# Kernel tuning notes

Measured on AMD Instinct MI355X. Metric: run time of the kernel, lower is better.

The kernel has to match this reference:

```python
import jax, jax.numpy as jnp
import numpy as np

N_NODES = 100000
N_EDGES = 2000000
EPS = 1e-8


def setup_inputs() -> dict:
    key = jax.random.key(0)
    k1, k2 = jax.random.split(key)
    node_positions = jax.random.normal(k1, (1, N_NODES, 2), dtype=jnp.float32) * 10.0
    adjacency = jnp.zeros((1, 1, 1), dtype=jnp.float32)  # unused by this axiom
    edge_index = jax.random.randint(k2, (2, N_EDGES), 0, N_NODES, dtype=jnp.int32)
    return {"node_positions": node_positions, "adjacency": adjacency, "edge_index": edge_index}


def reference(node_positions, adjacency, edge_index):
    """OrthogonalIntegrityAxiom loss.

    Mathematically identical to enumerating all intra-node edge pairs (i<j)
    and averaging cos^2(theta)*(1-cos^2(theta)) = dot^2 - dot^4 over pairs.
    Uses the moment identity: per node n with incident unit directions d_i,
      sum_{i,j} (d_i.d_j)^2 = ||sum_i d_i (x) d_i||_F^2
      sum_{i,j} (d_i.d_j)^4 = ||sum_i d_i^{(x)4}||_F^2
    Diagonal (i=j) terms equal 1 in both sums and cancel in the difference,
    so sum_{i<j} (dot^2 - dot^4) = (S2_n - S4_n)/2.
    """
    pos = node_positions.reshape(-1, 2)                      # (N, 2)
    n_total = pos.shape[0]
    src, dst = edge_index[0], edge_index[1]
    d = pos[dst] - pos[src]                                  # (E, 2)
    d = d / jnp.maximum(jnp.linalg.norm(d, axis=-1, keepdims=True), EPS)

    # Each edge is incident to both endpoints -> 2E (node, direction) pairs.
    nodes = jnp.concatenate([src, dst])                      # (2E,)
    dirs = jnp.concatenate([d, d], axis=0)                   # (2E, 2)

    o2 = (dirs[:, :, None] * dirs[:, None, :]).reshape(-1, 4)    # d (x) d, (2E, 4)
    o4 = (o2[:, :, None] * o2[:, None, :]).reshape(-1, 16)       # d^{(x)4}, (2E, 16)

    M = jax.ops.segment_sum(o2, nodes, num_segments=n_total)     # (N, 4)
    T = jax.ops.segment_sum(o4, nodes, num_segments=n_total)     # (N, 16)
    deg = jax.ops.segment_sum(jnp.ones_like(dirs[:, 0]), nodes, num_segments=n_total)

    S2 = jnp.sum(M * M, axis=-1)   # per-node sum_{i,j} (d_i.d_j)^2
    S4 = jnp.sum(T * T, axis=-1)   # per-node sum_{i,j} (d_i.d_j)^4

    pair_loss_sum = 0.5 * jnp.sum(S2 - S4)
    n_pairs = 0.5 * jnp.sum(deg * (deg - 1.0))
    loss = pair_loss_sum / jnp.maximum(n_pairs, 1.0)
    return loss
```

## Files before the change

### kernel.cpp

```cpp
#include <hip/hip_runtime.h>
#include <math.h>

#define EPSV 1e-8f

static constexpr double QC = 1.0 / 1024.0;
static constexpr double QS = 1.0 / 512.0;

static constexpr int BLOG = 8;
static constexpr int NPB = 1 << BLOG;
static constexpr int NBIN = 1024;
static constexpr int SRTN = 4096;
static constexpr int SDMAX = 2048;
static constexpr int NODE_BLOCKS = 256;

__device__ __forceinline__ unsigned int make_record(float dx, float dy) {
    float n2 = dx * dx + dy * dy;
    if (n2 > EPSV * EPSV) {
        float inv = 1.0f / n2;
        float c2 = (dx * dx - dy * dy) * inv;
        float s2 = (2.0f * dx * dy) * inv;
        float c4 = c2 * c2 - s2 * s2;
        float s4 = 2.0f * c2 * s2;
        c4 = fminf(fmaxf(c4, -1.0f), 1.0f);
        s4 = fminf(fmaxf(s4, -1.0f), 1.0f);
        unsigned int c4q = (unsigned int)__float2int_rn((c4 + 1.0f) * 1024.0f);
        unsigned int s4q = (unsigned int)__float2int_rn((s4 + 1.0f) * 512.0f);
        return (c4q << 11) | s4q;
    }
    return (1u << 31) | (1024u << 11) | 512u;
}

__device__ __forceinline__ unsigned long long rec_to_val(unsigned int r) {
    return (((unsigned long long)(r >> 31)) << 60) | (1ull << 52)
         | (((unsigned long long)((r >> 11) & 0xFFFu)) << 26)
         | (unsigned long long)(r & 0x7FFu);
}

__device__ __forceinline__ void decode_accum(unsigned long long a, double& pls, double& npr) {
    double s4sum = (double)(a & 0x3FFFFFFull);
    double c4sum = (double)((a >> 26) & 0x3FFFFFFull);
    double deg = (double)((a >> 52) & 0xFFull);
    double z = (double)(a >> 60);
    double u = deg - z;
    double C = c4sum * QC - deg;
    double S = s4sum * QS - deg;
    pls += (u * u - C * C - S * S) * 0.0625;
    npr += 0.5 * deg * (deg - 1.0);
}

__global__ __launch_bounds__(512, 8) void bin_kernel(
    const float2* __restrict__ pos,
    const int* __restrict__ ei,
    int E, int NB, int chunk, int rstride,
    unsigned short* __restrict__ ofs_out,
    unsigned int* __restrict__ buf)
{
    __shared__ __align__(16) unsigned int srt[SRTN];
    __shared__ __align__(16) int sdu[SDMAX];
    __shared__ __align__(16) int sdv[SDMAX];
    __shared__ unsigned int hist[512];
    __shared__ unsigned int scan[512];
    int blk = blockIdx.x;
    int t = threadIdx.x;
    int e0 = blk * chunk;
    int e1 = min(E, e0 + chunk);
    int cl = max(0, e1 - e0);
    const int* src = ei + e0;
    const int* dst = ei + E + e0;

    hist[t] = 0;
    __syncthreads();
    if (((E & 3) == 0)) {
        int nq = cl >> 2;
        for (int q = t; q < nq; q += 512) {
            int4 s4 = ((const int4*)src)[q];
            int4 d4 = ((const int4*)dst)[q];
            ((int4*)sdu)[q] = s4;
            ((int4*)sdv)[q] = d4;
            atomicAdd(&hist[s4.x >> BLOG], 1u);
            atomicAdd(&hist[s4.y >> BLOG], 1u);
            atomicAdd(&hist[s4.z >> BLOG], 1u);
            atomicAdd(&hist[s4.w >> BLOG], 1u);
            atomicAdd(&hist[d4.x >> BLOG], 1u);
            atomicAdd(&hist[d4.y >> BLOG], 1u);
            atomicAdd(&hist[d4.z >> BLOG], 1u);
            atomicAdd(&hist[d4.w >> BLOG], 1u);
        }
    } else {
        for (int i = t; i < cl; i += 512) {
            int s = src[i], d = dst[i];
            sdu[i] = s; sdv[i] = d;
            atomicAdd(&hist[s >> BLOG], 1u);
            atomicAdd(&hist[d >> BLOG], 1u);
        }
    }
    __syncthreads();
    scan[t] = hist[t];
    __syncthreads();
    for (int d = 1; d < 512; d <<= 1) {
        unsigned a = scan[t] + ((t >= d) ? scan[t - d] : 0u);
        __syncthreads();
        scan[t] = a;
        __syncthreads();
    }
    unsigned ex = scan[t] - hist[t];
    size_t row = (size_t)blk * (size_t)(NB + 1);
    if (t < NB) ofs_out[row + t] = (unsigned short)ex;
    if (t == 0) ofs_out[row + NB] = (unsigned short)(2 * cl);
    __syncthreads();
    hist[t] = ex;
    __syncthreads();
    for (int i = t; i < cl; i += 512) {
        int s = sdu[i], d = sdv[i];
        float2 ps = pos[s], pd = pos[d];
        unsigned int rec = make_record(pd.x - ps.x, pd.y - ps.y);
        unsigned is = atomicAdd(&hist[s >> BLOG], 1u);
        srt[is] = rec | ((unsigned)(s & (NPB - 1)) << 23);
        unsigned it = atomicAdd(&hist[d >> BLOG], 1u);
        srt[it] = rec | ((unsigned)(d & (NPB - 1)) << 23);
    }
    __syncthreads();
    unsigned int* dstb = buf + (size_t)blk * (size_t)rstride;
    int nrec = 2 * cl;
    if ((nrec & 3) == 0) {
        int nv = nrec >> 2;
        for (int i = t; i < nv; i += 512)
            ((uint4*)dstb)[i] = ((const uint4*)srt)[i];
    } else {
        for (int i = t; i < nrec; i += 512) dstb[i] = srt[i];
    }
}

__global__ __launch_bounds__(512) void bucket_kernel(
    const unsigned int* __restrict__ buf,
    const unsigned short* __restrict__ ofs,
    int rstride, int NB, int nbin,
    double* __restrict__ partials)
{
    __shared__ unsigned long long acc[8][NPB];
    __shared__ unsigned int so0[NBIN], so1[NBIN];
    __shared__ double sha[8], shb[8];
    int b = blockIdx.x;
    int t = threadIdx.x;
    int wid = t >> 6;
    for (int i = t; i < 8 * NPB; i += 512)
        ((unsigned long long*)acc)[i] = 0ull;
    for (int i = t; i < nbin; i += 512) {
        size_t row = (size_t)i * (size_t)(NB + 1);
        so0[i] = ofs[row + b];
        so1[i] = ofs[row + b + 1];
    }
    __syncthreads();

    int g = t >> 4;
    int l = t & 15;
    for (int rr = g; rr < nbin; rr += 32) {
        unsigned o0 = so0[rr], o1 = so1[rr];
        const unsigned int* p = buf + (size_t)rr * (size_t)rstride;
        for (unsigned i = o0 + l; i < o1; i += 16) {
            unsigned r = p[i];
            unsigned id = (r >> 23) & (NPB - 1);
            atomicAdd(&acc[wid][id], rec_to_val(r));
        }
    }
    __syncthreads();

    double pls = 0.0, npr = 0.0;
    for (int i = t; i < NPB; i += 512) {
        unsigned long long a = 0ull;
        #pragma unroll
        for (int w = 0; w < 8; ++w) a += acc[w][i];
        decode_accum(a, pls, npr);
    }
    for (int off = 32; off > 0; off >>= 1) {
        pls += __shfl_down(pls, off, 64);
        npr += __shfl_down(npr, off, 64);
    }
    int lane = t & 63;
    if (lane == 0) { sha[wid] = pls; shb[wid] = npr; }
    __syncthreads();
    if (t == 0) {
        double a = 0.0, c = 0.0;
        #pragma unroll
        for (int w = 0; w < 8; ++w) { a += sha[w]; c += shb[w]; }
        partials[2 * b + 0] = a;
        partials[2 * b + 1] = c;
    }
}

__global__ __launch_bounds__(256) void final_kernel(
    const double* __restrict__ partials,
    float* __restrict__ out,
    int nb)
{
    double pls = 0.0, npr = 0.0;
    for (int i = threadIdx.x; i < nb; i += blockDim.x) {
        pls += partials[2 * i + 0];
        npr += partials[2 * i + 1];
    }
    __shared__ double sha[4], shb[4];
    for (int off = 32; off > 0; off >>= 1) {
        pls += __shfl_down(pls, off, 64);
        npr += __shfl_down(npr, off, 64);
    }
    int lane = threadIdx.x & 63;
    int wid = threadIdx.x >> 6;
    if (lane == 0) { sha[wid] = pls; shb[wid] = npr; }
    __syncthreads();
    if (threadIdx.x == 0) {
        double a = sha[0] + sha[1] + sha[2] + sha[3];
        double b = shb[0] + shb[1] + shb[2] + shb[3];
        out[0] = (float)(a / fmax(b, 1.0));
    }
}

__global__ __launch_bounds__(256) void edge_kernel_fb(
    const float2* __restrict__ pos,
    const int* __restrict__ ei,
    unsigned long long* __restrict__ acc,
    int E)
{
    int tid = blockIdx.x * blockDim.x + threadIdx.x;
    int nthreads = gridDim.x * blockDim.x;
    const int* src = ei;
    const int* dst = ei + E;
    for (int e = tid; e < E; e += nthreads) {
        int s = src[e], t = dst[e];
        float2 ps = pos[s], pt = pos[t];
        unsigned long long val = rec_to_val(make_record(pt.x - ps.x, pt.y - ps.y));
        atomicAdd(&acc[s], val);
        atomicAdd(&acc[t], val);
    }
}

__global__ __launch_bounds__(256) void node_kernel_fb(
    const unsigned long long* __restrict__ acc,
    double* __restrict__ partials,
    int N)
{
    int tid = blockIdx.x * blockDim.x + threadIdx.x;
    int nthreads = gridDim.x * blockDim.x;
    double pls = 0.0, npr = 0.0;
    for (int n = tid; n < N; n += nthreads)
        decode_accum(acc[n], pls, npr);
    __shared__ double sha[4], shb[4];
    for (int off = 32; off > 0; off >>= 1) {
        pls += __shfl_down(pls, off, 64);
        npr += __shfl_down(npr, off, 64);
    }
    int lane = threadIdx.x & 63;
    int wid = threadIdx.x >> 6;
    if (lane == 0) { sha[wid] = pls; shb[wid] = npr; }
    __syncthreads();
    if (threadIdx.x == 0) {
        partials[2 * blockIdx.x + 0] = sha[0] + sha[1] + sha[2] + sha[3];
        partials[2 * blockIdx.x + 1] = shb[0] + shb[1] + shb[2] + shb[3];
    }
}

extern "C" void kernel_launch(void* const* d_in, const int* in_sizes, int n_in,
                              void* d_out, int out_size, void* d_ws, size_t ws_size,
                              hipStream_t stream) {
    const float* pos = (const float*)d_in[0];
    const int* ei = (const int*)d_in[2];
    int N = in_sizes[0] / 2;
    int E = in_sizes[2] / 2;
    float* out = (float*)d_out;

    int NB = (N + NPB - 1) >> BLOG;
    int chunk = ((E + NBIN - 1) / NBIN + 7) & ~7;
    int nrec_max = 2 * chunk;
    int rstride = (nrec_max + 15) & ~15;

    size_t off_buf = (size_t)NB * 16;
    size_t off_ofs = off_buf + (size_t)NBIN * (size_t)rstride * 4;
    size_t need = off_ofs + (size_t)NBIN * (size_t)(NB + 1) * 2;

    if (ws_size >= need && chunk <= SDMAX && nrec_max <= SRTN
        && NB + 1 <= 512 && nrec_max < 65536) {
        double* partials = (double*)d_ws;
        unsigned int* buf = (unsigned int*)((char*)d_ws + off_buf);
        unsigned short* ofs = (unsigned short*)((char*)d_ws + off_ofs);

        bin_kernel<<<NBIN, 512, 0, stream>>>(
            (const float2*)pos, ei, E, NB, chunk, rstride, ofs, buf);
        bucket_kernel<<<NB, 512, 0, stream>>>(buf, ofs, rstride, NB, NBIN, partials);
        final_kernel<<<1, 256, 0, stream>>>(partials, out, NB);
    } else {
        unsigned long long* acc = (unsigned long long*)d_ws;
        double* partials = (double*)((char*)d_ws + (size_t)N * 8);
        hipMemsetAsync(d_ws, 0, (size_t)N * 8 + (size_t)NODE_BLOCKS * 16, stream);
        int eb = min((E + 255) / 256, 2048);
        edge_kernel_fb<<<eb, 256, 0, stream>>>((const float2*)pos, ei, acc, E);
        node_kernel_fb<<<NODE_BLOCKS, 256, 0, stream>>>(acc, partials, N);
        final_kernel<<<1, 256, 0, stream>>>(partials, out, NODE_BLOCKS);
    }
}
```

Baseline: 110.0 us.

## Split per-edge record computation into separate gather kernel before binning

```diff
diff --git a/kernel.cpp b/kernel.cpp
--- a/kernel.cpp
+++ b/kernel.cpp
@@ -8,9 +8,9 @@
 
 static constexpr int BLOG = 8;
 static constexpr int NPB = 1 << BLOG;
-static constexpr int NBIN = 1024;
-static constexpr int SRTN = 4096;
-static constexpr int SDMAX = 2048;
+static constexpr int NBIN = 512;
+static constexpr int SRTN = 8192;
+static constexpr int SDMAX = 4096;
 static constexpr int NODE_BLOCKS = 256;
 
 __device__ __forceinline__ unsigned int make_record(float dx, float dy) {
@@ -48,9 +48,37 @@
     npr += 0.5 * deg * (deg - 1.0);
 }
 
-__global__ __launch_bounds__(512, 8) void bin_kernel(
+__global__ __launch_bounds__(256) void rec_kernel(
     const float2* __restrict__ pos,
     const int* __restrict__ ei,
+    unsigned int* __restrict__ recs,
+    int E)
+{
+    int tid = blockIdx.x * blockDim.x + threadIdx.x;
+    int nth = gridDim.x * blockDim.x;
+    const int* src = ei;
+    const int* dst = ei + E;
+    int nq = E >> 2;
+    for (int q = tid; q < nq; q += nth) {
+        int4 s4 = ((const int4*)src)[q];
+        int4 d4 = ((const int4*)dst)[q];
+        float2 a, b;
+        uint4 r;
+        a = pos[s4.x]; b = pos[d4.x]; r.x = make_record(b.x - a.x, b.y - a.y);
+        a = pos[s4.y]; b = pos[d4.y]; r.y = make_record(b.x - a.x, b.y - a.y);
+        a = pos[s4.z]; b = pos[d4.z]; r.z = make_record(b.x - a.x, b.y - a.y);
+        a = pos[s4.w]; b = pos[d4.w]; r.w = make_record(b.x - a.x, b.y - a.y);
+        ((uint4*)recs)[q] = r;
+    }
+    for (int e = (nq << 2) + tid; e < E; e += nth) {
+        float2 a = pos[src[e]], b = pos[dst[e]];
+        recs[e] = make_record(b.x - a.x, b.y - a.y);
+    }
+}
+
+__global__ __launch_bounds__(512, 8) void bin_kernel(
+    const int* __restrict__ ei,
+    const unsigned int* __restrict__ recs,
     int E, int NB, int chunk, int rstride,
     unsigned short* __restrict__ ofs_out,
     unsigned int* __restrict__ buf)
@@ -67,6 +95,7 @@
     int cl = max(0, e1 - e0);
     const int* src = ei + e0;
     const int* dst = ei + E + e0;
+    const unsigned int* rin = recs + e0;
 
     hist[t] = 0;
     __syncthreads();
@@ -110,14 +139,31 @@
     __syncthreads();
     hist[t] = ex;
     __syncthreads();
-    for (int i = t; i < cl; i += 512) {
-        int s = sdu[i], d = sdv[i];
-        float2 ps = pos[s], pd = pos[d];
-        unsigned int rec = make_record(pd.x - ps.x, pd.y - ps.y);
-        unsigned is = atomicAdd(&hist[s >> BLOG], 1u);
-        srt[is] = rec | ((unsigned)(s & (NPB - 1)) << 23);
-        unsigned it = atomicAdd(&hist[d >> BLOG], 1u);
-        srt[it] = rec | ((unsigned)(d & (NPB - 1)) << 23);
+    if (((E & 3) == 0)) {
+        int nq = cl >> 2;
+        for (int q = t; q < nq; q += 512) {
+            uint4 r4 = ((const uint4*)rin)[q];
+            int4 s4 = ((const int4*)sdu)[q];
+            int4 d4 = ((const int4*)sdv)[q];
+            unsigned c;
+            c = atomicAdd(&hist[s4.x >> BLOG], 1u); srt[c] = r4.x | ((unsigned)(s4.x & (NPB - 1)) << 23);
+            c = atomicAdd(&hist[d4.x >> BLOG], 1u); srt[c] = r4.x | ((unsigned)(d4.x & (NPB - 1)) << 23);
+            c = atomicAdd(&hist[s4.y >> BLOG], 1u); srt[c] = r4.y | ((unsigned)(s4.y & (NPB - 1)) << 23);
+            c = atomicAdd(&hist[d4.y >> BLOG], 1u); srt[c] = r4.y | ((unsigned)(d4.y & (NPB - 1)) << 23);
+            c = atomicAdd(&hist[s4.z >> BLOG], 1u); srt[c] = r4.z | ((unsigned)(s4.z & (NPB - 1)) << 23);
+            c = atomicAdd(&hist[d4.z >> BLOG], 1u); srt[c] = r4.z | ((unsigned)(d4.z & (NPB - 1)) << 23);
+            c = atomicAdd(&hist[s4.w >> BLOG], 1u); srt[c] = r4.w | ((unsigned)(s4.w & (NPB - 1)) << 23);
+            c = atomicAdd(&hist[d4.w >> BLOG], 1u); srt[c] = r4.w | ((unsigned)(d4.w & (NPB - 1)) << 23);
+        }
+    } else {
+        for (int i = t; i < cl; i += 512) {
+            int s = sdu[i], d = sdv[i];
+            unsigned int rec = rin[i];
+            unsigned is = atomicAdd(&hist[s >> BLOG], 1u);
+            srt[is] = rec | ((unsigned)(s & (NPB - 1)) << 23);
+            unsigned it = atomicAdd(&hist[d >> BLOG], 1u);
+            srt[it] = rec | ((unsigned)(d & (NPB - 1)) << 23);
+        }
     }
     __syncthreads();
     unsigned int* dstb = buf + (size_t)blk * (size_t)rstride;
@@ -274,16 +320,21 @@
 
     size_t off_buf = (size_t)NB * 16;
     size_t off_ofs = off_buf + (size_t)NBIN * (size_t)rstride * 4;
-    size_t need = off_ofs + (size_t)NBIN * (size_t)(NB + 1) * 2;
+    size_t off_rec = (off_ofs + (size_t)NBIN * (size_t)(NB + 1) * 2 + 15) & ~(size_t)15;
+    size_t need = off_rec + (size_t)E * 4;
 
     if (ws_size >= need && chunk <= SDMAX && nrec_max <= SRTN
         && NB + 1 <= 512 && nrec_max < 65536) {
         double* partials = (double*)d_ws;
         unsigned int* buf = (unsigned int*)((char*)d_ws + off_buf);
         unsigned short* ofs = (unsigned short*)((char*)d_ws + off_ofs);
-
+        unsigned int* recs = (unsigned int*)((char*)d_ws + off_rec);
+
+        int nq = (E >> 2) > 0 ? (E >> 2) : 1;
+        int rb = min((nq + 255) / 256, 4096);
+        rec_kernel<<<rb, 256, 0, stream>>>((const float2*)pos, ei, recs, E);
         bin_kernel<<<NBIN, 512, 0, stream>>>(
-            (const float2*)pos, ei, E, NB, chunk, rstride, ofs, buf);
+            ei, recs, E, NB, chunk, rstride, ofs, buf);
         bucket_kernel<<<NB, 512, 0, stream>>>(buf, ofs, rstride, NB, NBIN, partials);
         final_kernel<<<1, 256, 0, stream>>>(partials, out, NB);
     } else {
```

After: 114.3 us. 1.04x slower.

## Fuse final reduction into bucket kernel, use wave-shuffle scan, halve bin count

Applied to the files above, without the earlier changes.

```diff
diff --git a/kernel.cpp b/kernel.cpp
--- a/kernel.cpp
+++ b/kernel.cpp
@@ -8,9 +8,9 @@
 
 static constexpr int BLOG = 8;
 static constexpr int NPB = 1 << BLOG;
-static constexpr int NBIN = 1024;
-static constexpr int SRTN = 4096;
-static constexpr int SDMAX = 2048;
+static constexpr int NBIN = 512;
+static constexpr int SRTN = 8192;
+static constexpr int SDMAX = 4096;
 static constexpr int NODE_BLOCKS = 256;
 
 __device__ __forceinline__ unsigned int make_record(float dx, float dy) {
@@ -48,20 +48,22 @@
     npr += 0.5 * deg * (deg - 1.0);
 }
 
-__global__ __launch_bounds__(512, 8) void bin_kernel(
+__global__ __launch_bounds__(512) void bin_kernel(
     const float2* __restrict__ pos,
     const int* __restrict__ ei,
     int E, int NB, int chunk, int rstride,
     unsigned short* __restrict__ ofs_out,
-    unsigned int* __restrict__ buf)
+    unsigned int* __restrict__ buf,
+    unsigned long long* __restrict__ hdr)
 {
     __shared__ __align__(16) unsigned int srt[SRTN];
     __shared__ __align__(16) int sdu[SDMAX];
     __shared__ __align__(16) int sdv[SDMAX];
     __shared__ unsigned int hist[512];
-    __shared__ unsigned int scan[512];
+    __shared__ unsigned int wsum[8];
     int blk = blockIdx.x;
     int t = threadIdx.x;
+    if (blk == 0 && t < 4) hdr[t] = 0ull;
     int e0 = blk * chunk;
     int e1 = min(E, e0 + chunk);
     int cl = max(0, e1 - e0);
@@ -95,15 +97,20 @@
         }
     }
     __syncthreads();
-    scan[t] = hist[t];
-    __syncthreads();
-    for (int d = 1; d < 512; d <<= 1) {
-        unsigned a = scan[t] + ((t >= d) ? scan[t - d] : 0u);
-        __syncthreads();
-        scan[t] = a;
-        __syncthreads();
-    }
-    unsigned ex = scan[t] - hist[t];
+    int lane = t & 63, w = t >> 6;
+    unsigned v = hist[t];
+    unsigned sc = v;
+    #pragma unroll
+    for (int d = 1; d < 64; d <<= 1) {
+        unsigned n = __shfl_up(sc, d, 64);
+        if (lane >= d) sc += n;
+    }
+    if (lane == 63) wsum[w] = sc;
+    __syncthreads();
+    unsigned woff = 0;
+    #pragma unroll
+    for (int i = 0; i < 8; ++i) woff += (i < w) ? wsum[i] : 0u;
+    unsigned ex = woff + sc - v;
     size_t row = (size_t)blk * (size_t)(NB + 1);
     if (t < NB) ofs_out[row + t] = (unsigned short)ex;
     if (t == 0) ofs_out[row + NB] = (unsigned short)(2 * cl);
@@ -135,7 +142,8 @@
     const unsigned int* __restrict__ buf,
     const unsigned short* __restrict__ ofs,
     int rstride, int NB, int nbin,
-    double* __restrict__ partials)
+    unsigned long long* __restrict__ hdr,
+    float* __restrict__ out)
 {
     __shared__ unsigned long long acc[8][NPB];
     __shared__ unsigned int so0[NBIN], so1[NBIN];
@@ -183,8 +191,17 @@
         double a = 0.0, c = 0.0;
         #pragma unroll
         for (int w = 0; w < 8; ++w) { a += sha[w]; c += shb[w]; }
-        partials[2 * b + 0] = a;
-        partials[2 * b + 1] = c;
+        double* gs = (double*)hdr;
+        double r0 = atomicAdd(&gs[0], a);
+        double r1 = atomicAdd(&gs[1], c);
+        asm volatile("" :: "v"(r0), "v"(r1));
+        __threadfence();
+        unsigned long long cnt = atomicAdd(&hdr[2], 1ull);
+        if (cnt == (unsigned long long)(gridDim.x - 1)) {
+            double ta = atomicAdd(&gs[0], 0.0);
+            double tb = atomicAdd(&gs[1], 0.0);
+            out[0] = (float)(ta / fmax(tb, 1.0));
+        }
     }
 }
 
@@ -272,20 +289,19 @@
     int nrec_max = 2 * chunk;
     int rstride = (nrec_max + 15) & ~15;
 
-    size_t off_buf = (size_t)NB * 16;
+    size_t off_buf = 64;
     size_t off_ofs = off_buf + (size_t)NBIN * (size_t)rstride * 4;
     size_t need = off_ofs + (size_t)NBIN * (size_t)(NB + 1) * 2;
 
     if (ws_size >= need && chunk <= SDMAX && nrec_max <= SRTN
         && NB + 1 <= 512 && nrec_max < 65536) {
-        double* partials = (double*)d_ws;
+        unsigned long long* hdr = (unsigned long long*)d_ws;
         unsigned int* buf = (unsigned int*)((char*)d_ws + off_buf);
         unsigned short* ofs = (unsigned short*)((char*)d_ws + off_ofs);
 
         bin_kernel<<<NBIN, 512, 0, stream>>>(
-            (const float2*)pos, ei, E, NB, chunk, rstride, ofs, buf);
-        bucket_kernel<<<NB, 512, 0, stream>>>(buf, ofs, rstride, NB, NBIN, partials);
-        final_kernel<<<1, 256, 0, stream>>>(partials, out, NB);
+            (const float2*)pos, ei, E, NB, chunk, rstride, ofs, buf, hdr);
+        bucket_kernel<<<NB, 512, 0, stream>>>(buf, ofs, rstride, NB, NBIN, hdr, out);
     } else {
         unsigned long long* acc = (unsigned long long*)d_ws;
         double* partials = (double*)((char*)d_ws + (size_t)N * 8);
```

After: 118.4 us. 7.6% more time.
